# Performance work log

Hardware: AMD Instinct MI355X
Metric: run time of the kernel (lower is better)

Reference implementation:

```python
import jax, jax.numpy as jnp
import numpy as np

VOCAB = 23      # prime -> all nonzero scales invertible mod VOCAB
LEN = 256
BATCH = 512
HIDDEN = 4096
TEMP = 0.1


def _inv_table(v):
    # multiplicative inverse table mod v; inv(0) := 0 (non-invertible element)
    return np.array([0] + [pow(a, -1, v) for a in range(1, v)], dtype=np.int32)


def st_one_hot_argmax(x, temperature):
    """Straight-through one-hot argmax with tempered-softmax gradient."""
    soft = jax.nn.softmax(x / temperature, axis=-1)
    hard = jax.nn.one_hot(jnp.argmax(x, axis=-1), x.shape[-1], dtype=x.dtype)
    return soft + jax.lax.stop_gradient(hard - soft)


def one_hot_minus(inputs, shift):
    """(inputs - shift) % V in one-hot space via circular convolution."""
    V = inputs.shape[-1]
    # shift_matrix[..., u, v] = shift[..., (v - u) % V]  (== roll(shift, u))
    idx = (jnp.arange(V)[None, :] - jnp.arange(V)[:, None]) % V  # [u, v]
    shift_matrix = shift[..., idx]                               # [..., u, v]
    return jnp.einsum('...v,...uv->...u', inputs, shift_matrix)


def one_hot_multiply(inputs, scale):
    """(inputs * scale) % V in one-hot space; scale=0 component is dropped."""
    V = inputs.shape[-1]
    perm = (jnp.arange(V)[:, None] * jnp.arange(V)[None, :]) % V  # [a, v]
    P = jax.nn.one_hot(perm, V, dtype=inputs.dtype)               # [a, v, u]
    scale0 = scale * (jnp.arange(V) != 0).astype(scale.dtype)     # zero a=0 row
    return jnp.einsum('...v,...a,avu->...u', inputs, scale0, P)


def multiplicative_inverse(scale, v):
    """One-hot multiplicative inverse mod v via constant lookup table."""
    Inv = jax.nn.one_hot(jnp.asarray(_inv_table(v)), v, dtype=scale.dtype)  # [a, u]
    return jnp.einsum('...a,au->...u', scale, Inv)


def setup_inputs() -> dict:
    key = jax.random.key(0)
    k1, k2, k3 = jax.random.split(key, 3)
    tokens = jax.random.randint(k1, (BATCH, LEN), 0, VOCAB)
    inputs = jax.nn.one_hot(tokens, VOCAB, dtype=jnp.float32)     # [B, L, V]
    mask = (jnp.arange(LEN) % 2).astype(jnp.float32)[:, None]     # [L, 1]
    s1 = 1.0 / np.sqrt(LEN * VOCAB)
    s2 = 1.0 / np.sqrt(HIDDEN)
    W1 = jax.random.normal(k2, (LEN * VOCAB, HIDDEN), dtype=jnp.float32) * s1
    b1 = jnp.zeros((HIDDEN,), dtype=jnp.float32)
    W2 = jax.random.normal(k3, (HIDDEN, LEN * 2 * VOCAB), dtype=jnp.float32) * s2
    b2 = jnp.zeros((LEN * 2 * VOCAB,), dtype=jnp.float32)
    return {"inputs": inputs, "mask": mask, "W1": W1, "b1": b1, "W2": W2, "b2": b2}


def reference(inputs, mask, W1, b1, W2, b2):
    B, L, V = inputs.shape
    masked_inputs = mask * inputs                                 # [B, L, V]
    # layer(mask * inputs): flatten -> MLP -> [B, L, 2V]
    h = jax.nn.relu(masked_inputs.reshape(B, L * V) @ W1 + b1)
    net = (h @ W2 + b2).reshape(B, L, 2 * V)
    loc, scale = net[..., :V], net[..., V:]
    loc = st_one_hot_argmax(loc, TEMP)
    scale = st_one_hot_argmax(scale, TEMP)
    inv_scale = multiplicative_inverse(scale, V)
    shifted = one_hot_minus(inputs, loc)
    masked_outputs = (1.0 - mask) * one_hot_multiply(shifted, inv_scale)
    return masked_inputs + masked_outputs
```

## Files before the change

### kernel.cpp

```cpp
#include <hip/hip_runtime.h>
#include <cstddef>
#include <cstdint>

#define VOC 23
#define SEQ 256
#define NB  512
#define HID 4096
#define NCOL 11776
#define NPK 5888
#define KP  12288
#define EPS_TIE 4e-5f

__constant__ int INV23[VOC] = {0,1,12,8,6,14,4,10,3,18,7,21,2,16,5,20,13,19,9,17,15,11,22};

typedef __attribute__((ext_vector_type(8))) short short8;
typedef __attribute__((ext_vector_type(4))) float f32x4;

static __device__ __forceinline__ unsigned int f2bf(float f) {
  unsigned int x = __float_as_uint(f);
  return (x + 0x7fffu + ((x >> 16) & 1u)) >> 16;
}
static __device__ __forceinline__ float bf2f(unsigned int u) {
  return __uint_as_float(u << 16);
}

#define GL2LDS(g, l) __builtin_amdgcn_global_load_lds(                      \
    (const __attribute__((address_space(1))) unsigned int*)(g),             \
    (__attribute__((address_space(3))) unsigned int*)(l), 16, 0, 0)

__global__ __launch_bounds__(256) void k_tok_copy(const float* __restrict__ in,
                                                  float* __restrict__ out,
                                                  int* __restrict__ tok) {
  const int b = blockIdx.x;
  const int l = threadIdx.x;
  const float* row = in + ((size_t)b * SEQ + l) * VOC;
  int t = 0; float best = -1.0f;
#pragma unroll
  for (int v = 0; v < VOC; ++v) { float x = row[v]; if (x > best) { best = x; t = v; } }
  tok[b * SEQ + l] = t;
  if (l & 1) {
    float* o = out + ((size_t)b * SEQ + l) * VOC;
#pragma unroll
    for (int v = 0; v < VOC; ++v) o[v] = row[v];
  }
}

__global__ __launch_bounds__(256) void k_pack_w2(const float* __restrict__ W2,
                                                 unsigned short* __restrict__ Bp) {
  const int k0 = blockIdx.x * 64;
  const int j0 = blockIdx.y * 64;
  const int tid = threadIdx.x;
  __shared__ float T[64 * 65];
#pragma unroll
  for (int it = 0; it < 16; ++it) {
    int idx = it * 256 + tid;
    int k_l = idx >> 6, j_l = idx & 63;
    int j = j0 + j_l;
    int ee = j / 46, cc = j - ee * 46;
    T[j_l * 65 + k_l] = W2[(size_t)(k0 + k_l) * NCOL + 92 * ee + cc];
  }
  __syncthreads();
  const int j_l = tid >> 2, qt = tid & 3;
  unsigned int d[24];
#pragma unroll
  for (int pr = 0; pr < 8; ++pr) {
    int k_l = qt * 16 + pr * 2;
    float va = T[j_l * 65 + k_l], vb = T[j_l * 65 + k_l + 1];
    unsigned int ha = f2bf(va), la = f2bf(va - bf2f(ha));
    unsigned int hb = f2bf(vb), lb = f2bf(vb - bf2f(hb));
    d[pr * 3 + 0] = ha | (la << 16);
    d[pr * 3 + 1] = ha | (hb << 16);
    d[pr * 3 + 2] = lb | (hb << 16);
  }
  char* dst = ((char*)Bp) + (size_t)(j0 + j_l) * (KP * 2) + 6 * k0 + 96 * qt;
#pragma unroll
  for (int u = 0; u < 6; ++u) {
    uint4 w = make_uint4(d[4 * u], d[4 * u + 1], d[4 * u + 2], d[4 * u + 3]);
    ((uint4*)dst)[u] = w;
  }
}

__global__ __launch_bounds__(256) void k_hidden(const float* __restrict__ W1,
                                                const float* __restrict__ b1,
                                                const int* __restrict__ tok,
                                                float* __restrict__ h,
                                                unsigned short* __restrict__ Ap) {
  const int b = blockIdx.x;
  const int tid = threadIdx.x;
  __shared__ int rowS[128];
  if (tid < 128) {
    const int l = 2 * tid + 1;
    rowS[tid] = l * VOC + tok[b * SEQ + l];
  }
  __syncthreads();
  float4 acc[4];
#pragma unroll
  for (int j = 0; j < 4; ++j) acc[j] = make_float4(0.f, 0.f, 0.f, 0.f);
  for (int i = 0; i < 128; i += 2) {
    const float4* wr0 = (const float4*)(W1 + (size_t)rowS[i] * HID);
    const float4* wr1 = (const float4*)(W1 + (size_t)rowS[i + 1] * HID);
    float4 w0[4], w1[4];
#pragma unroll
    for (int j = 0; j < 4; ++j) w0[j] = wr0[tid + 256 * j];
#pragma unroll
    for (int j = 0; j < 4; ++j) w1[j] = wr1[tid + 256 * j];
#pragma unroll
    for (int j = 0; j < 4; ++j) {
      acc[j].x += w0[j].x; acc[j].y += w0[j].y; acc[j].z += w0[j].z; acc[j].w += w0[j].w;
      acc[j].x += w1[j].x; acc[j].y += w1[j].y; acc[j].z += w1[j].z; acc[j].w += w1[j].w;
    }
  }
  float4* hb = (float4*)(h + (size_t)b * HID);
  const float4* bv = (const float4*)b1;
#pragma unroll
  for (int j = 0; j < 4; ++j) {
    float4 bb = bv[tid + 256 * j];
    float4 r;
    r.x = fmaxf(acc[j].x + bb.x, 0.f);
    r.y = fmaxf(acc[j].y + bb.y, 0.f);
    r.z = fmaxf(acc[j].z + bb.z, 0.f);
    r.w = fmaxf(acc[j].w + bb.w, 0.f);
    hb[tid + 256 * j] = r;
    unsigned int h0 = f2bf(r.x), L0 = f2bf(r.x - bf2f(h0));
    unsigned int h1 = f2bf(r.y), L1 = f2bf(r.y - bf2f(h1));
    unsigned int h2 = f2bf(r.z), L2 = f2bf(r.z - bf2f(h2));
    unsigned int h3 = f2bf(r.w), L3 = f2bf(r.w - bf2f(h3));
    uint2* ap = (uint2*)(((char*)Ap) + (size_t)b * (KP * 2) + 24 * (tid + 256 * j));
    ap[0] = make_uint2(h0 | (h0 << 16), L0 | (h1 << 16));
    ap[1] = make_uint2(h1 | (L1 << 16), h2 | (h2 << 16));
    ap[2] = make_uint2(L2 | (h3 << 16), h3 | (L3 << 16));
  }
}

__global__ __launch_bounds__(256) void k3_mfma(const unsigned short* __restrict__ Ap,
                                               const unsigned short* __restrict__ Bp,
                                               float* __restrict__ partial) {
  __shared__ unsigned short Asm[128 * 64];
  __shared__ unsigned short Bsm[128 * 64];
  const int tid = threadIdx.x;
  const int bn0 = blockIdx.x * 128;
  const int bm0 = blockIdx.y * 128;
  const int s   = blockIdx.z;
  const int lane = tid & 63, wave = tid >> 6;
  const int wm = wave & 1, wn = wave >> 1;
  const int r = lane & 15, q = lane >> 4;

  f32x4 acc[4][4];
#pragma unroll
  for (int i = 0; i < 4; ++i)
#pragma unroll
    for (int j = 0; j < 4; ++j) acc[i][j] = (f32x4){0.f, 0.f, 0.f, 0.f};

  const int kb_base = s * 3072 * 2;
  for (int it = 0; it < 48; ++it) {
    __syncthreads();
    const int kb = kb_base + it * 128;
#pragma unroll
    for (int c2 = 0; c2 < 4; ++c2) {
      const int byte = c2 * 4096 + tid * 16;
      const int row = byte >> 7, col = byte & 127;
      GL2LDS(((const char*)Ap) + (size_t)(bm0 + row) * (KP * 2) + kb + col,
             ((char*)Asm) + byte);
      GL2LDS(((const char*)Bp) + (size_t)(bn0 + row) * (KP * 2) + kb + col,
             ((char*)Bsm) + byte);
    }
    __syncthreads();
#pragma unroll
    for (int kk = 0; kk < 2; ++kk) {
      short8 a[4], bfr[4];
#pragma unroll
      for (int i = 0; i < 4; ++i)
        a[i] = *(const short8*)((const char*)Asm + (64 * wm + 16 * i + r) * 128 + kk * 64 + q * 16);
#pragma unroll
      for (int j = 0; j < 4; ++j)
        bfr[j] = *(const short8*)((const char*)Bsm + (64 * wn + 16 * j + r) * 128 + kk * 64 + q * 16);
#pragma unroll
      for (int i = 0; i < 4; ++i)
#pragma unroll
        for (int j = 0; j < 4; ++j)
          acc[i][j] = __builtin_amdgcn_mfma_f32_16x16x32_bf16(a[i], bfr[j], acc[i][j], 0, 0, 0);
    }
  }
  float* pbase = partial + (size_t)s * NB * NPK;
#pragma unroll
  for (int i = 0; i < 4; ++i) {
    const int m = bm0 + 64 * wm + 16 * i + 4 * q;
#pragma unroll
    for (int j = 0; j < 4; ++j) {
      const int n = bn0 + 64 * wn + 16 * j + r;
      float* pp = pbase + (size_t)m * NPK + n;
#pragma unroll
      for (int reg = 0; reg < 4; ++reg)
        pp[(size_t)reg * NPK] = acc[i][j][reg];
    }
  }
}

__global__ __launch_bounds__(256) void k_epilogue(const float* __restrict__ partial,
                                                  const float* __restrict__ b2,
                                                  const int* __restrict__ tok,
                                                  int* __restrict__ win,
                                                  int* __restrict__ gcnt,
                                                  int* __restrict__ glist,
                                                  float* __restrict__ out) {
  const int b = blockIdx.x, tid = threadIdx.x;
  const int e = tid >> 1, grp = tid & 1;
  __shared__ int winS[256];
  __shared__ int flagS[256];
  float x[VOC];
  const size_t base = (size_t)b * NPK + 46 * e + 23 * grp;
#pragma unroll
  for (int c = 0; c < VOC; ++c) x[c] = b2[92 * e + 23 * grp + c];
#pragma unroll
  for (int s2 = 0; s2 < 4; ++s2) {
    const float* pp = partial + (size_t)s2 * NB * NPK + base;
#pragma unroll
    for (int c = 0; c < VOC; ++c) x[c] += pp[c];
  }
  float b0 = -1e30f, b1v = -1e30f; int bi = 0;
#pragma unroll
  for (int c = 0; c < VOC; ++c) {
    if (x[c] > b0) { b1v = b0; b0 = x[c]; bi = c; }
    else if (x[c] > b1v) b1v = x[c];
  }
  winS[tid] = bi;
  flagS[tid] = (b0 - b1v < EPS_TIE) ? 1 : 0;
  __syncthreads();
  if (!grp) {
    const int loc = winS[tid], sc = winS[tid + 1];
    win[b * 256 + 2 * e] = loc;
    win[b * 256 + 2 * e + 1] = sc;
    const int f0 = flagS[tid], f1 = flagS[tid + 1];
    if (f0 | f1) {
      int idx = atomicAdd(gcnt, 1);
      glist[idx] = e | (b << 7) | (f0 << 16) | (f1 << 17);
    }
    const int l = 2 * e;
    float* o = out + ((size_t)b * SEQ + l) * VOC;
    if (sc == 0) {
      for (int v = 0; v < VOC; ++v) o[v] = 0.f;
    } else {
      const int t = tok[b * SEQ + l];
      int dd = t - loc; if (dd < 0) dd += VOC;
      const int u = (INV23[sc] * dd) % VOC;
      for (int v = 0; v < VOC; ++v) o[v] = (v == u) ? 1.f : 0.f;
    }
  }
}

__global__ __launch_bounds__(192) void k_recheck(const float* __restrict__ h,
                                                 const float* __restrict__ W2,
                                                 const float* __restrict__ b2,
                                                 const int* __restrict__ tok,
                                                 const int* __restrict__ win,
                                                 const int* __restrict__ gcnt,
                                                 const int* __restrict__ glist,
                                                 float* __restrict__ out) {
  const int tid = threadIdx.x;
  __shared__ double dpart[184];
  __shared__ double dlog[VOC];
  __shared__ int decS[2];
  const int n = gcnt[0];
  for (int ei = blockIdx.x; ei < n; ei += 128) {
    const int ent = glist[ei];
    const int e = ent & 127, b = (ent >> 7) & 511;
    const int l = 2 * e;
#pragma unroll
    for (int grp = 0; grp < 2; ++grp) {
      if (!(ent & (1 << (16 + grp)))) {
        if (tid == 0) decS[grp] = win[b * 256 + 2 * e + grp];
      } else {
        const int col0 = 92 * e + 23 * grp;
        if (tid < 184) {
          const int c = tid >> 3, part = tid & 7;
          const float* hb = h + (size_t)b * HID;
          const size_t colc = (size_t)(col0 + c);
          double sacc[8] = {0, 0, 0, 0, 0, 0, 0, 0};
          const int kbase = part * 512;
          for (int kk = 0; kk < 512; kk += 8) {
#pragma unroll
            for (int t2 = 0; t2 < 8; ++t2) {
              const int k = kbase + kk + t2;
              sacc[t2] += (double)hb[k] * (double)W2[(size_t)k * NCOL + colc];
            }
          }
          dpart[tid] = ((sacc[0] + sacc[1]) + (sacc[2] + sacc[3])) +
                       ((sacc[4] + sacc[5]) + (sacc[6] + sacc[7]));
        }
        __syncthreads();
        if (tid < VOC) {
          double sd = (double)b2[col0 + tid];
#pragma unroll
          for (int p2 = 0; p2 < 8; ++p2) sd += dpart[tid * 8 + p2];
          dlog[tid] = sd;
        }
        __syncthreads();
        if (tid == 0) {
          double best = -1e300; int bi2 = 0;
#pragma unroll
          for (int c = 0; c < VOC; ++c)
            if (dlog[c] > best) { best = dlog[c]; bi2 = c; }
          decS[grp] = bi2;
        }
      }
      __syncthreads();
    }
    if (tid < VOC) {
      const int loc = decS[0], sc = decS[1];
      float val = 0.f;
      if (sc != 0) {
        const int t = tok[b * SEQ + l];
        int dd = t - loc; if (dd < 0) dd += VOC;
        const int u = (INV23[sc] * dd) % VOC;
        val = (tid == u) ? 1.f : 0.f;
      }
      out[((size_t)b * SEQ + l) * VOC + tid] = val;
    }
    __syncthreads();
  }
}

extern "C" void kernel_launch(void* const* d_in, const int* in_sizes, int n_in,
                              void* d_out, int out_size, void* d_ws, size_t ws_size,
                              hipStream_t stream) {
  const float* in  = (const float*)d_in[0];
  const float* W1  = (const float*)d_in[2];
  const float* b1  = (const float*)d_in[3];
  const float* W2  = (const float*)d_in[4];
  const float* b2  = (const float*)d_in[5];
  float* out = (float*)d_out;

  char* w = (char*)d_ws;
  int* tok = (int*)w;                         w += (size_t)NB * SEQ * 4;
  float* h = (float*)w;                       w += (size_t)NB * HID * 4;
  unsigned short* Ap = (unsigned short*)w;    w += (size_t)NB * KP * 2;
  unsigned short* Bp = (unsigned short*)w;    w += (size_t)NPK * KP * 2;
  float* partial = (float*)w;                 w += (size_t)4 * NB * NPK * 4;
  int* win = (int*)w;                         w += (size_t)NB * 256 * 4;
  int* gcnt = (int*)w;                        w += 256;
  int* glist = (int*)w;                       w += (size_t)65536 * 4;

  k_tok_copy<<<dim3(NB), dim3(256), 0, stream>>>(in, out, tok);
  k_pack_w2<<<dim3(64, 92), dim3(256), 0, stream>>>(W2, Bp);
  k_hidden<<<dim3(NB), dim3(256), 0, stream>>>(W1, b1, tok, h, Ap);
  hipMemsetAsync(gcnt, 0, 4, stream);
  k3_mfma<<<dim3(46, 4, 4), dim3(256), 0, stream>>>(Ap, Bp, partial);
  k_epilogue<<<dim3(NB), dim3(256), 0, stream>>>(partial, b2, tok, win, gcnt, glist, out);
  k_recheck<<<dim3(128), dim3(192), 0, stream>>>(h, W2, b2, tok, win, gcnt, glist, out);
}
```

Before: 680.5 us.

## Double-buffer LDS tiles with XOR swizzle and XCD-aware block remapping in MFMA GEMM

The bf16 MFMA GEMM kernel now stages 32-wide K tiles into two LDS buffers. The global-to-LDS load of the next tile is issued before computing on the current one, removing one barrier per step and overlapping load latency with MFMA work. LDS placement uses an XOR swizzle across 16-byte chunks to reduce bank conflicts on the fragment reads. The 3D grid is flattened and remapped so that neighbouring blocks, which share A/B panels, land together on the same XCD for better L2 reuse. Costs are more address math, a fixed swizzle layout tied to the 128x64-byte tile shape, and a remap formula hardcoded to 736 blocks.

Result: slower. 699.8 us (+2.8%).

```diff
diff --git a/kernel.cpp b/kernel.cpp
--- a/kernel.cpp
+++ b/kernel.cpp
@@ -132,55 +132,85 @@
   }
 }
 
+#define STAGE(bufA, bufB, kbv) do {                                               \
+    _Pragma("unroll")                                                             \
+    for (int c_ = 0; c_ < 2; ++c_) {                                              \
+      GL2LDS(((const char*)Ap) + aG[c_] + (kbv), ((char*)(bufA)) + ldsOff[c_]);   \
+      GL2LDS(((const char*)Bp) + bG[c_] + (kbv), ((char*)(bufB)) + ldsOff[c_]);   \
+    }                                                                             \
+  } while (0)
+
+#define COMPUTE(bufA, bufB) do {                                                  \
+    short8 a_[4], b_[4];                                                          \
+    _Pragma("unroll")                                                             \
+    for (int i_ = 0; i_ < 4; ++i_)                                                \
+      a_[i_] = *(const short8*)((const char*)(bufA) + aoff + 1024 * i_);          \
+    _Pragma("unroll")                                                             \
+    for (int j_ = 0; j_ < 4; ++j_)                                                \
+      b_[j_] = *(const short8*)((const char*)(bufB) + boff + 1024 * j_);          \
+    _Pragma("unroll")                                                             \
+    for (int i_ = 0; i_ < 4; ++i_)                                                \
+      _Pragma("unroll")                                                           \
+      for (int j_ = 0; j_ < 4; ++j_)                                              \
+        acc[i_][j_] = __builtin_amdgcn_mfma_f32_16x16x32_bf16(a_[i_], b_[j_],     \
+                                                              acc[i_][j_], 0, 0, 0); \
+  } while (0)
+
 __global__ __launch_bounds__(256) void k3_mfma(const unsigned short* __restrict__ Ap,
                                                const unsigned short* __restrict__ Bp,
                                                float* __restrict__ partial) {
-  __shared__ unsigned short Asm[128 * 64];
-  __shared__ unsigned short Bsm[128 * 64];
+  __shared__ unsigned short AsmD[2][128 * 32];
+  __shared__ unsigned short BsmD[2][128 * 32];
   const int tid = threadIdx.x;
-  const int bn0 = blockIdx.x * 128;
-  const int bm0 = blockIdx.y * 128;
-  const int s   = blockIdx.z;
+
+  const int f = blockIdx.x;
+  const int nf = (f & 7) * 92 + (f >> 3);
+  const int bn0 = (nf >> 4) * 128;
+  const int inner = nf & 15;
+  const int bm0 = (inner & 3) * 128;
+  const int s = inner >> 2;
+
   const int lane = tid & 63, wave = tid >> 6;
   const int wm = wave & 1, wn = wave >> 1;
   const int r = lane & 15, q = lane >> 4;
 
+  size_t aG[2], bG[2]; int ldsOff[2];
+#pragma unroll
+  for (int c = 0; c < 2; ++c) {
+    const int G = c * 256 + tid;
+    const int line = G >> 3, gph = G & 7;
+    const int gin = gph ^ (line & 7);
+    const int grow = 2 * line + (gin >> 2);
+    const int gcol = (gin & 3) << 4;
+    aG[c] = (size_t)(bm0 + grow) * (KP * 2) + gcol;
+    bG[c] = (size_t)(bn0 + grow) * (KP * 2) + gcol;
+    ldsOff[c] = G * 16;
+  }
+
+  const int gphR = (((((r & 1) << 2) | q) ^ ((r >> 1) & 7)) << 4);
+  const int aoff = (32 * wm + (r >> 1)) * 128 + gphR;
+  const int boff = (32 * wn + (r >> 1)) * 128 + gphR;
+
   f32x4 acc[4][4];
 #pragma unroll
   for (int i = 0; i < 4; ++i)
 #pragma unroll
     for (int j = 0; j < 4; ++j) acc[i][j] = (f32x4){0.f, 0.f, 0.f, 0.f};
 
-  const int kb_base = s * 3072 * 2;
-  for (int it = 0; it < 48; ++it) {
+  const int kb0 = s * 6144;
+  STAGE(AsmD[0], BsmD[0], kb0);
+  __syncthreads();
+#pragma unroll 1
+  for (int it = 0; it < 96; it += 2) {
+    const int kb = kb0 + it * 64;
+    STAGE(AsmD[1], BsmD[1], kb + 64);
+    COMPUTE(AsmD[0], BsmD[0]);
     __syncthreads();
-    const int kb = kb_base + it * 128;
-#pragma unroll
-    for (int c2 = 0; c2 < 4; ++c2) {
-      const int byte = c2 * 4096 + tid * 16;
-      const int row = byte >> 7, col = byte & 127;
-      GL2LDS(((const char*)Ap) + (size_t)(bm0 + row) * (KP * 2) + kb + col,
-             ((char*)Asm) + byte);
-      GL2LDS(((const char*)Bp) + (size_t)(bn0 + row) * (KP * 2) + kb + col,
-             ((char*)Bsm) + byte);
-    }
+    if (it < 94) STAGE(AsmD[0], BsmD[0], kb + 128);
+    COMPUTE(AsmD[1], BsmD[1]);
     __syncthreads();
-#pragma unroll
-    for (int kk = 0; kk < 2; ++kk) {
-      short8 a[4], bfr[4];
-#pragma unroll
-      for (int i = 0; i < 4; ++i)
-        a[i] = *(const short8*)((const char*)Asm + (64 * wm + 16 * i + r) * 128 + kk * 64 + q * 16);
-#pragma unroll
-      for (int j = 0; j < 4; ++j)
-        bfr[j] = *(const short8*)((const char*)Bsm + (64 * wn + 16 * j + r) * 128 + kk * 64 + q * 16);
-#pragma unroll
-      for (int i = 0; i < 4; ++i)
-#pragma unroll
-        for (int j = 0; j < 4; ++j)
-          acc[i][j] = __builtin_amdgcn_mfma_f32_16x16x32_bf16(a[i], bfr[j], acc[i][j], 0, 0, 0);
-    }
-  }
+  }
+
   float* pbase = partial + (size_t)s * NB * NPK;
 #pragma unroll
   for (int i = 0; i < 4; ++i) {
@@ -344,7 +374,7 @@
   k_pack_w2<<<dim3(64, 92), dim3(256), 0, stream>>>(W2, Bp);
   k_hidden<<<dim3(NB), dim3(256), 0, stream>>>(W1, b1, tok, h, Ap);
   hipMemsetAsync(gcnt, 0, 4, stream);
-  k3_mfma<<<dim3(46, 4, 4), dim3(256), 0, stream>>>(Ap, Bp, partial);
+  k3_mfma<<<dim3(736), dim3(256), 0, stream>>>(Ap, Bp, partial);
   k_epilogue<<<dim3(NB), dim3(256), 0, stream>>>(partial, b2, tok, win, gcnt, glist, out);
   k_recheck<<<dim3(128), dim3(192), 0, stream>>>(h, W2, b2, tok, win, gcnt, glist, out);
 }
```
